# Optimization experiments

Hardware: AMD Instinct MI355X
Metric: run time of the kernel (lower is better)

## Reference

```python
import jax, jax.numpy as jnp
import numpy as np

B, L, D = 8, 4096, 768


def setup_inputs() -> dict:
    key = jax.random.key(0)
    k1, = jax.random.split(key, 1)
    x = jax.random.normal(k1, (B, L, D), dtype=jnp.float32)
    alpha = jnp.ones((L, 1), dtype=jnp.float32)  # nn.Parameter(torch.ones(l_dim, 1))
    return {"x": x, "alpha": alpha}


def reference(x, alpha):
    # Original: y = (x @ x^T).mean(-1, keepdim=True) / D
    # Algebraically identical (mean over j of sum_d x_i,d x_j,d = x_i . mean_j x_j):
    d = x.shape[-1]
    l = x.shape[1]
    mean_x = jnp.mean(x, axis=1)                       # [B, D]
    y = jnp.einsum('bld,bd->bl', x, mean_x)[..., None] / d  # [B, L, 1]
    # Original: y = (y @ y^T).mean(-1, keepdim=True) / L
    # (y y^T)_ij = y_i * y_j; mean over j = y_i * mean(y)
    y = y * jnp.mean(y, axis=1, keepdims=True) / l     # [B, L, 1]
    # y * x + alpha  (alpha broadcast over batch and D); dropout p=0 -> identity
    return alpha + y * x
```

## Files before the change

### kernel.cpp

```cpp
#include <hip/hip_runtime.h>

constexpr int Bn = 8;
constexpr int Ln = 4096;
constexpr int Dn = 768;
constexpr int CHUNKS = 64;
constexpr int RPC = Ln / CHUNKS;

__global__ void k_colsum_part(const float* __restrict__ x, float4* __restrict__ part) {
    int b = blockIdx.x / CHUNKS;
    int c = blockIdx.x % CHUNKS;
    int t = threadIdx.x;
    const float4* xb = (const float4*)(x + ((size_t)b * Ln + (size_t)c * RPC) * Dn);
    float4 s = {0.f, 0.f, 0.f, 0.f};
    for (int l = 0; l < RPC; ++l) {
        float4 v = xb[(size_t)l * (Dn / 4) + t];
        s.x += v.x; s.y += v.y; s.z += v.z; s.w += v.w;
    }
    part[((size_t)b * CHUNKS + c) * (Dn / 4) + t] = s;
}

__global__ void k_scale(const float* __restrict__ part, float* __restrict__ m) {
    int b = blockIdx.x;
    int t = threadIdx.x;
    const float* pb = part + (size_t)b * CHUNKS * Dn;
    float s0 = 0.f, s1 = 0.f, s2 = 0.f;
    for (int c = 0; c < CHUNKS; ++c) {
        const float* row = pb + (size_t)c * Dn;
        s0 += row[t];
        s1 += row[t + 256];
        s2 += row[t + 512];
    }
    float ssq = s0 * s0 + s1 * s1 + s2 * s2;
    #pragma unroll
    for (int off = 1; off < 64; off <<= 1) ssq += __shfl_xor(ssq, off);
    __shared__ float wsum[4];
    int wave = t >> 6, lane = t & 63;
    if (lane == 0) wsum[wave] = ssq;
    __syncthreads();
    float ss = wsum[0] + wsum[1] + wsum[2] + wsum[3];

    const float f1 = 1.0f / ((float)Ln * (float)Dn);
    float scale = ss * f1 * f1 / ((float)Ln * (float)Ln);
    m[b * Dn + t]       = s0 * scale;
    m[b * Dn + t + 256] = s1 * scale;
    m[b * Dn + t + 512] = s2 * scale;
}

__global__ void k_fused(const float* __restrict__ x, const float* __restrict__ m,
                        const float* __restrict__ alpha, float* __restrict__ out) {
    int wave = threadIdx.x >> 6;
    int lane = threadIdx.x & 63;
    int row  = blockIdx.x * 4 + wave;
    int b    = row >> 12;
    int l    = row & (Ln - 1);

    const float4* xr = (const float4*)(x + (size_t)row * Dn);
    const float4* mr = (const float4*)(m + (size_t)b * Dn);

    float4 x0 = xr[lane], x1 = xr[lane + 64], x2 = xr[lane + 128];
    float4 m0 = mr[lane], m1 = mr[lane + 64], m2 = mr[lane + 128];

    float acc = x0.x * m0.x + x0.y * m0.y + x0.z * m0.z + x0.w * m0.w
              + x1.x * m1.x + x1.y * m1.y + x1.z * m1.z + x1.w * m1.w
              + x2.x * m2.x + x2.y * m2.y + x2.z * m2.z + x2.w * m2.w;
    #pragma unroll
    for (int off = 1; off < 64; off <<= 1) acc += __shfl_xor(acc, off);

    float a = alpha[l];
    float4* orow = (float4*)(out + (size_t)row * Dn);
    float4 o0 = {a + acc * x0.x, a + acc * x0.y, a + acc * x0.z, a + acc * x0.w};
    float4 o1 = {a + acc * x1.x, a + acc * x1.y, a + acc * x1.z, a + acc * x1.w};
    float4 o2 = {a + acc * x2.x, a + acc * x2.y, a + acc * x2.z, a + acc * x2.w};
    orow[lane]       = o0;
    orow[lane + 64]  = o1;
    orow[lane + 128] = o2;
}

extern "C" void kernel_launch(void* const* d_in, const int* in_sizes, int n_in,
                              void* d_out, int out_size, void* d_ws, size_t ws_size,
                              hipStream_t stream) {
    const float* x     = (const float*)d_in[0];
    const float* alpha = (const float*)d_in[1];
    float* out = (float*)d_out;

    float* part = (float*)d_ws;
    float* m    = part + (size_t)Bn * CHUNKS * Dn;

    k_colsum_part<<<Bn * CHUNKS, 192, 0, stream>>>(x, (float4*)part);
    k_scale<<<Bn, 256, 0, stream>>>(part, m);
    k_fused<<<(Bn * Ln) / 4, 256, 0, stream>>>(x, m, alpha, out);
}
```

Before: 197.1 us.

## Fuse three kernels into one cooperative kernel with grid syncs and L2 reuse

Replaces the colsum, scale and apply kernels with a single cooperative kernel of 512 blocks that uses grid.sync between phases. Each block reads the same 64-row chunk in phase 1 and phase 3, so the second read may hit in cache, and two kernel launches are removed. In exchange the kernel pays for two grid-wide barriers and runs phase 2 on only 8 blocks while the others wait. Phase 3 also has far fewer blocks than the old 8192-block apply kernel.

```diff
diff --git a/kernel.cpp b/kernel.cpp
--- a/kernel.cpp
+++ b/kernel.cpp
@@ -1,79 +1,93 @@
 #include <hip/hip_runtime.h>
+#include <hip/hip_cooperative_groups.h>
+
+namespace cg = cooperative_groups;
 
 constexpr int Bn = 8;
 constexpr int Ln = 4096;
 constexpr int Dn = 768;
-constexpr int CHUNKS = 64;
-constexpr int RPC = Ln / CHUNKS;
+constexpr int CPB  = 64;
+constexpr int NBLK = Bn * CPB;
+constexpr int RPB  = Ln / CPB;
 
-__global__ void k_colsum_part(const float* __restrict__ x, float4* __restrict__ part) {
-    int b = blockIdx.x / CHUNKS;
-    int c = blockIdx.x % CHUNKS;
-    int t = threadIdx.x;
-    const float4* xb = (const float4*)(x + ((size_t)b * Ln + (size_t)c * RPC) * Dn);
-    float4 s = {0.f, 0.f, 0.f, 0.f};
-    for (int l = 0; l < RPC; ++l) {
-        float4 v = xb[(size_t)l * (Dn / 4) + t];
-        s.x += v.x; s.y += v.y; s.z += v.z; s.w += v.w;
+__global__ void __launch_bounds__(256, 2)
+k_all(const float* __restrict__ x, const float* __restrict__ alpha,
+      float* __restrict__ out, float* __restrict__ part, float* __restrict__ m) {
+    cg::grid_group grid = cg::this_grid();
+    __shared__ float wsum[4];
+
+    const int b = blockIdx.x >> 6;
+    const int c = blockIdx.x & 63;
+    const int t = threadIdx.x;
+    const int wave = t >> 6, lane = t & 63;
+
+    {
+        const float* xb = x + ((size_t)b * Ln + (size_t)c * RPB) * Dn;
+        float s0 = 0.f, s1 = 0.f, s2 = 0.f;
+        for (int l = 0; l < RPB; ++l) {
+            const float* row = xb + (size_t)l * Dn;
+            s0 += row[t];
+            s1 += row[t + 256];
+            s2 += row[t + 512];
+        }
+        float* pr = part + (size_t)blockIdx.x * Dn;
+        pr[t]       = s0;
+        pr[t + 256] = s1;
+        pr[t + 512] = s2;
     }
-    part[((size_t)b * CHUNKS + c) * (Dn / 4) + t] = s;
-}
+    grid.sync();
 
-__global__ void k_scale(const float* __restrict__ part, float* __restrict__ m) {
-    int b = blockIdx.x;
-    int t = threadIdx.x;
-    const float* pb = part + (size_t)b * CHUNKS * Dn;
-    float s0 = 0.f, s1 = 0.f, s2 = 0.f;
-    for (int c = 0; c < CHUNKS; ++c) {
-        const float* row = pb + (size_t)c * Dn;
-        s0 += row[t];
-        s1 += row[t + 256];
-        s2 += row[t + 512];
+    if (c == 0) {
+        const float* pb = part + (size_t)b * CPB * Dn;
+        float s0 = 0.f, s1 = 0.f, s2 = 0.f;
+        for (int k = 0; k < CPB; ++k) {
+            const float* row = pb + (size_t)k * Dn;
+            s0 += row[t];
+            s1 += row[t + 256];
+            s2 += row[t + 512];
+        }
+        float ssq = s0 * s0 + s1 * s1 + s2 * s2;
+        #pragma unroll
+        for (int off = 1; off < 64; off <<= 1) ssq += __shfl_xor(ssq, off);
+        if (lane == 0) wsum[wave] = ssq;
+        __syncthreads();
+        float ss = wsum[0] + wsum[1] + wsum[2] + wsum[3];
+
+        const float f1 = 1.0f / ((float)Ln * (float)Dn);
+        float scale = ss * f1 * f1 / ((float)Ln * (float)Ln);
+        m[b * Dn + t]       = s0 * scale;
+        m[b * Dn + t + 256] = s1 * scale;
+        m[b * Dn + t + 512] = s2 * scale;
     }
-    float ssq = s0 * s0 + s1 * s1 + s2 * s2;
-    #pragma unroll
-    for (int off = 1; off < 64; off <<= 1) ssq += __shfl_xor(ssq, off);
-    __shared__ float wsum[4];
-    int wave = t >> 6, lane = t & 63;
-    if (lane == 0) wsum[wave] = ssq;
-    __syncthreads();
-    float ss = wsum[0] + wsum[1] + wsum[2] + wsum[3];
+    grid.sync();
 
-    const float f1 = 1.0f / ((float)Ln * (float)Dn);
-    float scale = ss * f1 * f1 / ((float)Ln * (float)Ln);
-    m[b * Dn + t]       = s0 * scale;
-    m[b * Dn + t + 256] = s1 * scale;
-    m[b * Dn + t + 512] = s2 * scale;
-}
+    {
+        const float4* mr = (const float4*)(m + (size_t)b * Dn);
+        float4 m0 = mr[lane], m1 = mr[lane + 64], m2 = mr[lane + 128];
 
-__global__ void k_fused(const float* __restrict__ x, const float* __restrict__ m,
-                        const float* __restrict__ alpha, float* __restrict__ out) {
-    int wave = threadIdx.x >> 6;
-    int lane = threadIdx.x & 63;
-    int row  = blockIdx.x * 4 + wave;
-    int b    = row >> 12;
-    int l    = row & (Ln - 1);
+        const int row0 = b * Ln + c * RPB;
+        for (int r = wave; r < RPB; r += 4) {
+            int row = row0 + r;
+            int l   = c * RPB + r;
+            const float4* xr = (const float4*)(x + (size_t)row * Dn);
+            float4 x0 = xr[lane], x1 = xr[lane + 64], x2 = xr[lane + 128];
 
-    const float4* xr = (const float4*)(x + (size_t)row * Dn);
-    const float4* mr = (const float4*)(m + (size_t)b * Dn);
+            float acc = x0.x * m0.x + x0.y * m0.y + x0.z * m0.z + x0.w * m0.w
+                      + x1.x * m1.x + x1.y * m1.y + x1.z * m1.z + x1.w * m1.w
+                      + x2.x * m2.x + x2.y * m2.y + x2.z * m2.z + x2.w * m2.w;
+            #pragma unroll
+            for (int off = 1; off < 64; off <<= 1) acc += __shfl_xor(acc, off);
 
-    float4 x0 = xr[lane], x1 = xr[lane + 64], x2 = xr[lane + 128];
-    float4 m0 = mr[lane], m1 = mr[lane + 64], m2 = mr[lane + 128];
-
-    float acc = x0.x * m0.x + x0.y * m0.y + x0.z * m0.z + x0.w * m0.w
-              + x1.x * m1.x + x1.y * m1.y + x1.z * m1.z + x1.w * m1.w
-              + x2.x * m2.x + x2.y * m2.y + x2.z * m2.z + x2.w * m2.w;
-    #pragma unroll
-    for (int off = 1; off < 64; off <<= 1) acc += __shfl_xor(acc, off);
-
-    float a = alpha[l];
-    float4* orow = (float4*)(out + (size_t)row * Dn);
-    float4 o0 = {a + acc * x0.x, a + acc * x0.y, a + acc * x0.z, a + acc * x0.w};
-    float4 o1 = {a + acc * x1.x, a + acc * x1.y, a + acc * x1.z, a + acc * x1.w};
-    float4 o2 = {a + acc * x2.x, a + acc * x2.y, a + acc * x2.z, a + acc * x2.w};
-    orow[lane]       = o0;
-    orow[lane + 64]  = o1;
-    orow[lane + 128] = o2;
+            float a = alpha[l];
+            float4* orow = (float4*)(out + (size_t)row * Dn);
+            float4 o0 = {a + acc * x0.x, a + acc * x0.y, a + acc * x0.z, a + acc * x0.w};
+            float4 o1 = {a + acc * x1.x, a + acc * x1.y, a + acc * x1.z, a + acc * x1.w};
+            float4 o2 = {a + acc * x2.x, a + acc * x2.y, a + acc * x2.z, a + acc * x2.w};
+            orow[lane]       = o0;
+            orow[lane + 64]  = o1;
+            orow[lane + 128] = o2;
+        }
+    }
 }
 
 extern "C" void kernel_launch(void* const* d_in, const int* in_sizes, int n_in,
@@ -84,9 +98,8 @@
     float* out = (float*)d_out;
 
     float* part = (float*)d_ws;
-    float* m    = part + (size_t)Bn * CHUNKS * Dn;
+    float* m    = part + (size_t)NBLK * Dn;
 
-    k_colsum_part<<<Bn * CHUNKS, 192, 0, stream>>>(x, (float4*)part);
-    k_scale<<<Bn, 256, 0, stream>>>(part, m);
-    k_fused<<<(Bn * Ln) / 4, 256, 0, stream>>>(x, m, alpha, out);
+    void* args[] = {(void*)&x, (void*)&alpha, (void*)&out, (void*)&part, (void*)&m};
+    hipLaunchCooperativeKernel((void*)k_all, dim3(NBLK), dim3(256), args, 0, stream);
 }
```

New measurement: 306.3 us. 55.4% more time.
